# Kernel optimization log

Hardware: AMD Instinct MI355X
Metric: run time of the kernel (lower is better)

## Reference

```python
import jax, jax.numpy as jnp
import numpy as np

B, T, D_IN = 512, 128, 256
H1, H2 = 1024, 1024
LABEL_DIM = 3


def _lstm_layer(x, W, U, b):
    """Run one keras-LSTMCell layer over x: [T, B, D_in] -> [T, B, H].

    Keras gate order is (i, f, g, o); c' = f*c + i*tanh(g); h = o*tanh(c').
    """
    H = U.shape[0]
    batch = x.shape[1]

    def step(carry, xt):
        h, c = carry
        z = xt @ W + h @ U + b  # [B, 4H]
        i, f, g, o = jnp.split(z, 4, axis=-1)
        i = jax.nn.sigmoid(i)
        f = jax.nn.sigmoid(f)
        g = jnp.tanh(g)
        o = jax.nn.sigmoid(o)
        c_new = f * c + i * g
        h_new = o * jnp.tanh(c_new)
        return (h_new, c_new), h_new

    init = (jnp.zeros((batch, H), x.dtype), jnp.zeros((batch, H), x.dtype))
    _, hs = jax.lax.scan(step, init, x)
    return hs  # [T, B, H]


def setup_inputs() -> dict:
    key = jax.random.key(0)
    ks = jax.random.split(key, 10)
    chars = jax.random.normal(ks[0], (B, T, D_IN), dtype=jnp.float32)
    # sequence lengths in [1, T] so sequence_length - 1 is a valid index
    sequence_length = jax.random.randint(ks[1], (B,), 1, T + 1)
    s = 0.05
    W1 = jax.random.normal(ks[2], (D_IN, 4 * H1), dtype=jnp.float32) * s
    U1 = jax.random.normal(ks[3], (H1, 4 * H1), dtype=jnp.float32) * s
    b1 = jnp.zeros((4 * H1,), dtype=jnp.float32)
    W2 = jax.random.normal(ks[4], (H1, 4 * H2), dtype=jnp.float32) * s
    U2 = jax.random.normal(ks[5], (H2, 4 * H2), dtype=jnp.float32) * s
    b2 = jnp.zeros((4 * H2,), dtype=jnp.float32)
    Wd = jax.random.normal(ks[6], (H2, LABEL_DIM), dtype=jnp.float32) * s
    bd = jnp.zeros((LABEL_DIM,), dtype=jnp.float32)
    return {"chars": chars, "sequence_length": sequence_length,
            "W1": W1, "U1": U1, "b1": b1,
            "W2": W2, "U2": U2, "b2": b2,
            "Wd": Wd, "bd": bd}


def reference(chars, sequence_length, W1, U1, b1, W2, U2, b2, Wd, bd):
    # chars: [B, T, 256] -> time-major [T, B, 256]
    x = jnp.transpose(chars, (1, 0, 2))
    x = _lstm_layer(x, W1, U1, b1)          # [T, B, H1]
    x = _lstm_layer(x, W2, U2, b2)          # [T, B, H2]
    # gather the hidden state at the last valid timestep of each sequence
    batch = chars.shape[0]
    hidden = x[sequence_length - 1, jnp.arange(batch)]  # [B, H2]
    return jax.nn.relu(hidden @ Wd + bd)    # [B, label_dim]
```

## Files before the change

kernel.cpp:

```cpp
#include <hip/hip_runtime.h>
#include <hip/hip_bf16.h>


typedef __hip_bfloat16 bf16;
typedef __attribute__((ext_vector_type(8))) short bfrag8;
typedef __attribute__((ext_vector_type(4))) float accf4;

#define BATCH 512
#define TSTEPS 128
#define DIN 256
#define H 1024
#define NG 4096

__device__ __forceinline__ float sigm(float x) { return 1.0f / (1.0f + __expf(-x)); }
__device__ __forceinline__ float tanh_f(float x) {
    float a = fabsf(x);
    float e = __expf(-2.0f * a);
    float t = (1.0f - e) / (1.0f + e);
    return x < 0.0f ? -t : t;
}
__device__ __forceinline__ unsigned short bfr16(float x) {
    bf16 h = __float2bfloat16(x);
    return *(unsigned short*)&h;
}
__device__ __forceinline__ void gll16(const void* g, void* l) {
    __builtin_amdgcn_global_load_lds(
        (const __attribute__((address_space(1))) unsigned int*)g,
        (__attribute__((address_space(3))) unsigned int*)l, 16, 0, 0);
}

__global__ void k_repack(const float* __restrict__ W, const float* __restrict__ U,
                         bf16* __restrict__ Bp, int KIN)
{
    __shared__ float tile[128][65];
    int kt = blockIdx.x, nt = blockIdx.y;
    int lane = threadIdx.x;
    int n = nt * 64 + lane;
    int orig = ((n >> 4) & 3) * 1024 + (n >> 7) * 32 + ((n >> 6) & 1) * 16 + (n & 15);
    for (int j = 0; j < 128; ++j) {
        int k = kt * 128 + j;
        tile[j][lane] = (k < KIN) ? W[(size_t)k * NG + orig]
                                  : U[(size_t)(k - KIN) * NG + orig];
    }
    __syncthreads();
    for (int u = 0; u < 16; ++u) {
        int cid = u * 64 + lane;
        int nloc = cid >> 4;
        int pos = cid & 15;
        int nn = nt * 64 + nloc;
        int kc = pos ^ (nn & 7);
        alignas(16) unsigned short pk[8];
        #pragma unroll
        for (int jj = 0; jj < 8; ++jj) pk[jj] = bfr16(tile[kc * 8 + jj][nloc]);
        *(int4*)(Bp + ((size_t)kt * NG + nn) * 128 + pos * 8) = *(int4*)pk;
    }
}

__global__ void k_sort(const int* __restrict__ seqlen, int* __restrict__ perm,
                       int* __restrict__ cnt)
{
    __shared__ int hist[129];
    __shared__ int base[129];
    __shared__ int cur[129];
    int tid = threadIdx.x;
    if (tid < 129) { hist[tid] = 0; cur[tid] = 0; }
    __syncthreads();
    int len = seqlen[tid];
    atomicAdd(&hist[len], 1);
    __syncthreads();
    if (tid == 0) {
        int acc = 0;
        for (int l = 128; l >= 1; --l) { base[l] = acc; acc += hist[l]; }
        base[0] = acc;
    }
    __syncthreads();
    int pos = base[len] + atomicAdd(&cur[len], 1);
    perm[pos] = tid;
    if (tid < 128) cnt[tid] = base[tid];
}

struct StepJob {
    const float* Xf;
    const bf16* A0;
    const bf16* A1;
    const bf16* Bp;
    const float* bias;
    float* C;
    bf16* Hout;
    float* hidden;
    const int* seqlen;
    const int* perm;
    const int* cnt;
    int xstride;
    int ksplit;
    int KT;
    int t;
};

__global__ __launch_bounds__(256, 2) void k_step(StepJob j0, StepJob j1)
{
    __shared__ __align__(16) bf16 Alds[64 * 128];
    __shared__ __align__(16) bf16 Blds[128 * 128];

    int jidx = blockIdx.x >> 8;
    const StepJob jb = jidx ? j1 : j0;
    int bi = blockIdx.x & 255;
    int xcd = bi & 7;
    int s = bi >> 3;
    int btr = s >> 2;
    int btile = jidx ? (7 - btr) : btr;
    int ntile = ((s & 3) << 3) | xcd;
    int b0 = btile * 64;
    if (b0 >= jb.cnt[jb.t]) return;

    int tid = threadIdx.x;
    int wv = tid >> 6, lane = tid & 63;
    int n0 = ntile * 128;
    int mw = (wv & 1) * 32;
    int nw = (wv >> 1) * 64;
    int c = lane & 15, q = lane >> 4;

    const accf4 zero4 = {0.f, 0.f, 0.f, 0.f};
    accf4 acc[2][4];
    #pragma unroll
    for (int i = 0; i < 2; ++i)
        #pragma unroll
        for (int j = 0; j < 4; ++j) acc[i][j] = zero4;

    for (int kt = 0; kt < jb.KT; ++kt) {
        int k0 = kt << 7;
        if (jb.Xf && k0 < jb.ksplit) {
            #pragma unroll
            for (int uu = 0; uu < 4; ++uu) {
                int u = uu * 256 + tid;
                int r = u >> 4;
                int pos = u & 15;
                int kc = pos ^ (r & 7);
                const float* src = jb.Xf + (size_t)jb.perm[b0 + r] * jb.xstride + k0 + kc * 8;
                float4 va = *(const float4*)src;
                float4 vb = *(const float4*)(src + 4);
                alignas(16) unsigned short pk[8];
                pk[0] = bfr16(va.x); pk[1] = bfr16(va.y);
                pk[2] = bfr16(va.z); pk[3] = bfr16(va.w);
                pk[4] = bfr16(vb.x); pk[5] = bfr16(vb.y);
                pk[6] = bfr16(vb.z); pk[7] = bfr16(vb.w);
                *(int4*)((char*)Alds + u * 16) = *(int4*)pk;
            }
        } else {
            const bf16* Asrc; int kk0;
            if (k0 < jb.ksplit) { Asrc = jb.A0; kk0 = k0; }
            else                { Asrc = jb.A1; kk0 = k0 - jb.ksplit; }
            #pragma unroll
            for (int cc = 0; cc < 4; ++cc) {
                int ob = wv * 4096 + cc * 1024;
                int o = ob + lane * 16;
                int r = o >> 8;
                const char* g = (const char*)Asrc + (size_t)(b0 + r) * (H * 2) + kk0 * 2 + (o & 255);
                gll16(g, (char*)Alds + ob);
            }
        }
        const char* Bg = (const char*)jb.Bp + ((size_t)kt * NG + n0) * 256;
        #pragma unroll
        for (int cc = 0; cc < 8; ++cc) {
            int ob = wv * 8192 + cc * 1024;
            gll16(Bg + ob + lane * 16, (char*)Blds + ob);
        }
        __syncthreads();
        #pragma unroll
        for (int kk = 0; kk < 128; kk += 32) {
            int kc = (kk >> 3) + q;
            int ra = mw + c;
            int pa = (kc ^ (ra & 7)) << 3;
            bfrag8 af0 = *(const bfrag8*)(Alds + ra * 128 + pa);
            bfrag8 af1 = *(const bfrag8*)(Alds + (ra + 16) * 128 + pa);
            #pragma unroll
            for (int nt = 0; nt < 4; ++nt) {
                int nn = nw + nt * 16 + c;
                bfrag8 bfv = *(const bfrag8*)(Blds + nn * 128 + ((kc ^ (nn & 7)) << 3));
                acc[0][nt] = __builtin_amdgcn_mfma_f32_16x16x32_bf16(af0, bfv, acc[0][nt], 0, 0, 0);
                acc[1][nt] = __builtin_amdgcn_mfma_f32_16x16x32_bf16(af1, bfv, acc[1][nt], 0, 0, 0);
            }
        }
        __syncthreads();
    }

    int hcol = ntile * 32 + (wv >> 1) * 16 + c;
    float bi_ = jb.bias[hcol],         bf_ = jb.bias[H + hcol];
    float bg_ = jb.bias[2 * H + hcol], bo_ = jb.bias[3 * H + hcol];
    int seg = hcol & ~127;
    int kc_ = (hcol & 127) >> 3;
    int jl = hcol & 7;
    #pragma unroll
    for (int mt = 0; mt < 2; ++mt) {
        #pragma unroll
        for (int reg = 0; reg < 4; ++reg) {
            int b = b0 + mw + mt * 16 + q * 4 + reg;
            float ig = sigm(acc[mt][0][reg] + bi_);
            float fg = sigm(acc[mt][1][reg] + bf_);
            float gv = tanh_f(acc[mt][2][reg] + bg_);
            float og = sigm(acc[mt][3][reg] + bo_);
            size_t ci = (size_t)b * H + hcol;
            float cv = fg * jb.C[ci] + ig * gv;
            jb.C[ci] = cv;
            float h = og * tanh_f(cv);
            jb.Hout[(size_t)b * H + seg + ((kc_ ^ (b & 7)) << 3) + jl] = __float2bfloat16(h);
            if (jb.hidden) {
                int pb = jb.perm[b];
                if (jb.seqlen[pb] - 1 == jb.t)
                    jb.hidden[(size_t)pb * H + hcol] = h;
            }
        }
    }
}

__global__ void k_final(const float* __restrict__ hidden, const float* __restrict__ Wd,
                        const float* __restrict__ bd, float* __restrict__ out)
{
    int b = blockIdx.x;
    int l = threadIdx.x;
    float p0 = 0.f, p1 = 0.f, p2 = 0.f;
    for (int jj = l; jj < H; jj += 64) {
        float hv = hidden[(size_t)b * H + jj];
        p0 += hv * Wd[jj * 3 + 0];
        p1 += hv * Wd[jj * 3 + 1];
        p2 += hv * Wd[jj * 3 + 2];
    }
    #pragma unroll
    for (int off = 32; off > 0; off >>= 1) {
        p0 += __shfl_down(p0, off);
        p1 += __shfl_down(p1, off);
        p2 += __shfl_down(p2, off);
    }
    if (l == 0) {
        out[b * 3 + 0] = fmaxf(p0 + bd[0], 0.f);
        out[b * 3 + 1] = fmaxf(p1 + bd[1], 0.f);
        out[b * 3 + 2] = fmaxf(p2 + bd[2], 0.f);
    }
}

extern "C" void kernel_launch(void* const* d_in, const int* in_sizes, int n_in,
                              void* d_out, int out_size, void* d_ws, size_t ws_size,
                              hipStream_t stream)
{
    const float* chars = (const float*)d_in[0];
    const int* seqlen  = (const int*)d_in[1];
    const float* W1 = (const float*)d_in[2];
    const float* U1 = (const float*)d_in[3];
    const float* b1 = (const float*)d_in[4];
    const float* W2 = (const float*)d_in[5];
    const float* U2 = (const float*)d_in[6];
    const float* b2 = (const float*)d_in[7];
    const float* Wd = (const float*)d_in[8];
    const float* bd = (const float*)d_in[9];
    float* out = (float*)d_out;

    char* ws = (char*)d_ws;
    size_t off = 0;
    bf16* Bp1 = (bf16*)(ws + off); off += (size_t)10 * NG * 128 * 2;
    bf16* Bp2 = (bf16*)(ws + off); off += (size_t)16 * NG * 128 * 2;
    bf16* h1  = (bf16*)(ws + off); off += (size_t)2 * BATCH * H * 2;
    bf16* h2  = (bf16*)(ws + off); off += (size_t)2 * BATCH * H * 2;
    float* c1 = (float*)(ws + off); off += (size_t)BATCH * H * 4;
    float* c2 = (float*)(ws + off); off += (size_t)BATCH * H * 4;
    float* hidden = (float*)(ws + off); off += (size_t)BATCH * H * 4;
    int* perm = (int*)(ws + off); off += BATCH * 4;
    int* cntA = (int*)(ws + off); off += TSTEPS * 4;
    if (ws_size < off) return;

    hipMemsetAsync(h1, 0, (size_t)2 * BATCH * H * 2, stream);
    hipMemsetAsync(h2, 0, (size_t)2 * BATCH * H * 2, stream);
    hipMemsetAsync(c1, 0, (size_t)BATCH * H * 4, stream);
    hipMemsetAsync(c2, 0, (size_t)BATCH * H * 4, stream);

    k_repack<<<dim3(10, 64), 64, 0, stream>>>(W1, U1, Bp1, 256);
    k_repack<<<dim3(16, 64), 64, 0, stream>>>(W2, U2, Bp2, 1024);
    k_sort<<<1, 512, 0, stream>>>(seqlen, perm, cntA);

    const size_t HS = (size_t)BATCH * H;

    auto mkL1 = [&](int s) {
        StepJob J;
        J.Xf = chars + (size_t)s * DIN;  J.xstride = TSTEPS * DIN;
        J.A0 = nullptr;
        J.A1 = h1 + (size_t)((s + 1) & 1) * HS;
        J.Bp = Bp1; J.bias = b1; J.C = c1;
        J.Hout = h1 + (size_t)(s & 1) * HS;
        J.hidden = nullptr; J.seqlen = nullptr;
        J.perm = perm; J.cnt = cntA;
        J.ksplit = 256; J.KT = 10; J.t = s;
        return J;
    };
    auto mkL2 = [&](int s) {
        StepJob J;
        J.Xf = nullptr; J.xstride = 0;
        J.A0 = h1 + (size_t)(s & 1) * HS;
        J.A1 = h2 + (size_t)((s + 1) & 1) * HS;
        J.Bp = Bp2; J.bias = b2; J.C = c2;
        J.Hout = h2 + (size_t)(s & 1) * HS;
        J.hidden = hidden; J.seqlen = seqlen;
        J.perm = perm; J.cnt = cntA;
        J.ksplit = 1024; J.KT = 16; J.t = s;
        return J;
    };

    StepJob first = mkL1(0);
    k_step<<<256, 256, 0, stream>>>(first, first);
    for (int t = 0; t < TSTEPS - 1; ++t) {
        k_step<<<512, 256, 0, stream>>>(mkL2(t), mkL1(t + 1));
    }
    StepJob last = mkL2(TSTEPS - 1);
    k_step<<<256, 256, 0, stream>>>(last, last);
    k_final<<<512, 64, 0, stream>>>(hidden, Wd, bd, out);
}
```

Before: 3.756 ms.

## Replace per-timestep kernel launches with a persistent kernel and grid barrier

The 129 per-step launches become one persistent kernel of 512 blocks. Each block loops over timesteps and synchronises with the others through an atomic-counter grid barrier backed by agent-scope fences. This removes launch overhead and the kernel-boundary drain between steps. It depends on all 512 blocks being co-resident (two blocks per CU under the launch bounds), adds spin-wait cost, and has a guard that can break out of the barrier, which risks correctness if it fires.

```diff
diff --git a/kernel.cpp b/kernel.cpp
--- a/kernel.cpp
+++ b/kernel.cpp
@@ -11,6 +11,7 @@
 #define DIN 256
 #define H 1024
 #define NG 4096
+#define NBLK 512
 
 __device__ __forceinline__ float sigm(float x) { return 1.0f / (1.0f + __expf(-x)); }
 __device__ __forceinline__ float tanh_f(float x) {
@@ -90,36 +91,17 @@
     float* hidden;
     const int* seqlen;
     const int* perm;
-    const int* cnt;
     int xstride;
     int ksplit;
     int KT;
     int t;
 };
 
-__global__ __launch_bounds__(256, 2) void k_step(StepJob j0, StepJob j1)
-{
-    __shared__ __align__(16) bf16 Alds[64 * 128];
-    __shared__ __align__(16) bf16 Blds[128 * 128];
-
-    int jidx = blockIdx.x >> 8;
-    const StepJob jb = jidx ? j1 : j0;
-    int bi = blockIdx.x & 255;
-    int xcd = bi & 7;
-    int s = bi >> 3;
-    int btr = s >> 2;
-    int btile = jidx ? (7 - btr) : btr;
-    int ntile = ((s & 3) << 3) | xcd;
-    int b0 = btile * 64;
-    if (b0 >= jb.cnt[jb.t]) return;
-
-    int tid = threadIdx.x;
-    int wv = tid >> 6, lane = tid & 63;
-    int n0 = ntile * 128;
-    int mw = (wv & 1) * 32;
-    int nw = (wv >> 1) * 64;
-    int c = lane & 15, q = lane >> 4;
-
+__device__ __forceinline__ void step_body(
+    const StepJob& jb, bf16* Alds, bf16* Blds,
+    int b0, int n0, int ntile, int tid, int wv, int lane,
+    int mw, int nw, int c, int q, bool is_l2)
+{
     const accf4 zero4 = {0.f, 0.f, 0.f, 0.f};
     accf4 acc[2][4];
     #pragma unroll
@@ -204,11 +186,101 @@
             jb.C[ci] = cv;
             float h = og * tanh_f(cv);
             jb.Hout[(size_t)b * H + seg + ((kc_ ^ (b & 7)) << 3) + jl] = __float2bfloat16(h);
-            if (jb.hidden) {
+            if (is_l2) {
                 int pb = jb.perm[b];
                 if (jb.seqlen[pb] - 1 == jb.t)
                     jb.hidden[(size_t)pb * H + hcol] = h;
             }
+        }
+    }
+}
+
+struct PersistArgs {
+    const float* chars;
+    const int* seqlen;
+    const float* b1; const float* b2;
+    const bf16* Bp1; const bf16* Bp2;
+    float* c1; float* c2;
+    bf16* h1; bf16* h2;
+    float* hidden;
+    const int* perm; const int* cnt;
+    unsigned* bar;
+};
+
+__global__ __launch_bounds__(256, 2) void k_persist(PersistArgs P)
+{
+    __shared__ __align__(16) bf16 Alds[64 * 128];
+    __shared__ __align__(16) bf16 Blds[128 * 128];
+
+    int jidx = blockIdx.x >> 8;
+    int bi = blockIdx.x & 255;
+    int xcd = bi & 7;
+    int sl = bi >> 3;
+    int btr = sl >> 2;
+    int btile = jidx ? (7 - btr) : btr;
+    int ntile = ((sl & 3) << 3) | xcd;
+    int b0 = btile * 64;
+
+    int tid = threadIdx.x;
+    int wv = tid >> 6, lane = tid & 63;
+    int n0 = ntile * 128;
+    int mw = (wv & 1) * 32;
+    int nw = (wv >> 1) * 64;
+    int c = lane & 15, q = lane >> 4;
+    const size_t HS = (size_t)BATCH * H;
+
+    StepJob J;
+    J.perm = P.perm;
+    if (jidx == 1) {
+        J.Bp = P.Bp1; J.bias = P.b1; J.C = P.c1;
+        J.hidden = nullptr; J.seqlen = nullptr;
+        J.xstride = TSTEPS * DIN; J.ksplit = 256; J.KT = 10;
+    } else {
+        J.Bp = P.Bp2; J.bias = P.b2; J.C = P.c2;
+        J.hidden = P.hidden; J.seqlen = P.seqlen;
+        J.xstride = 0; J.ksplit = 1024; J.KT = 16;
+    }
+
+    for (int s = 0; s <= TSTEPS; ++s) {
+        bool active;
+        if (jidx == 0) {
+            active = (s >= 1);
+            int t = s - 1;
+            J.t = t;
+            J.Xf = nullptr;
+            J.A0 = P.h1 + (size_t)(t & 1) * HS;
+            J.A1 = P.h2 + (size_t)((t + 1) & 1) * HS;
+            J.Hout = P.h2 + (size_t)(t & 1) * HS;
+        } else {
+            active = (s < TSTEPS);
+            int t = s;
+            J.t = t;
+            J.Xf = P.chars + (size_t)t * DIN;
+            J.A0 = nullptr;
+            J.A1 = P.h1 + (size_t)((t + 1) & 1) * HS;
+            J.Hout = P.h1 + (size_t)(t & 1) * HS;
+        }
+        if (active && b0 < P.cnt[J.t]) {
+            step_body(J, Alds, Blds, b0, n0, ntile, tid, wv, lane, mw, nw, c, q,
+                      jidx == 0);
+        }
+
+        if (s < TSTEPS) {
+            __builtin_amdgcn_fence(__ATOMIC_RELEASE, "agent");
+            __syncthreads();
+            if (tid == 0) {
+                __hip_atomic_fetch_add(P.bar, 1u, __ATOMIC_RELAXED,
+                                       __HIP_MEMORY_SCOPE_AGENT);
+                unsigned target = (unsigned)(s + 1) * NBLK;
+                int guard = 0;
+                while (__hip_atomic_load(P.bar, __ATOMIC_RELAXED,
+                                         __HIP_MEMORY_SCOPE_AGENT) < target) {
+                    __builtin_amdgcn_s_sleep(1);
+                    if (++guard > 100000) break;
+                }
+            }
+            __syncthreads();
+            __builtin_amdgcn_fence(__ATOMIC_ACQUIRE, "agent");
         }
     }
 }
@@ -265,50 +337,29 @@
     float* hidden = (float*)(ws + off); off += (size_t)BATCH * H * 4;
     int* perm = (int*)(ws + off); off += BATCH * 4;
     int* cntA = (int*)(ws + off); off += TSTEPS * 4;
+    unsigned* bar = (unsigned*)(ws + off); off += 256;
     if (ws_size < off) return;
 
     hipMemsetAsync(h1, 0, (size_t)2 * BATCH * H * 2, stream);
     hipMemsetAsync(h2, 0, (size_t)2 * BATCH * H * 2, stream);
     hipMemsetAsync(c1, 0, (size_t)BATCH * H * 4, stream);
     hipMemsetAsync(c2, 0, (size_t)BATCH * H * 4, stream);
+    hipMemsetAsync(bar, 0, 256, stream);
 
     k_repack<<<dim3(10, 64), 64, 0, stream>>>(W1, U1, Bp1, 256);
     k_repack<<<dim3(16, 64), 64, 0, stream>>>(W2, U2, Bp2, 1024);
     k_sort<<<1, 512, 0, stream>>>(seqlen, perm, cntA);
 
-    const size_t HS = (size_t)BATCH * H;
-
-    auto mkL1 = [&](int s) {
-        StepJob J;
-        J.Xf = chars + (size_t)s * DIN;  J.xstride = TSTEPS * DIN;
-        J.A0 = nullptr;
-        J.A1 = h1 + (size_t)((s + 1) & 1) * HS;
-        J.Bp = Bp1; J.bias = b1; J.C = c1;
-        J.Hout = h1 + (size_t)(s & 1) * HS;
-        J.hidden = nullptr; J.seqlen = nullptr;
-        J.perm = perm; J.cnt = cntA;
-        J.ksplit = 256; J.KT = 10; J.t = s;
-        return J;
-    };
-    auto mkL2 = [&](int s) {
-        StepJob J;
-        J.Xf = nullptr; J.xstride = 0;
-        J.A0 = h1 + (size_t)(s & 1) * HS;
-        J.A1 = h2 + (size_t)((s + 1) & 1) * HS;
-        J.Bp = Bp2; J.bias = b2; J.C = c2;
-        J.Hout = h2 + (size_t)(s & 1) * HS;
-        J.hidden = hidden; J.seqlen = seqlen;
-        J.perm = perm; J.cnt = cntA;
-        J.ksplit = 1024; J.KT = 16; J.t = s;
-        return J;
-    };
-
-    StepJob first = mkL1(0);
-    k_step<<<256, 256, 0, stream>>>(first, first);
-    for (int t = 0; t < TSTEPS - 1; ++t) {
-        k_step<<<512, 256, 0, stream>>>(mkL2(t), mkL1(t + 1));
-    }
-    StepJob last = mkL2(TSTEPS - 1);
-    k_step<<<256, 256, 0, stream>>>(last, last);
+    PersistArgs P;
+    P.chars = chars; P.seqlen = seqlen;
+    P.b1 = b1; P.b2 = b2;
+    P.Bp1 = Bp1; P.Bp2 = Bp2;
+    P.c1 = c1; P.c2 = c2;
+    P.h1 = h1; P.h2 = h2;
+    P.hidden = hidden;
+    P.perm = perm; P.cnt = cntA;
+    P.bar = bar;
+    k_persist<<<dim3(NBLK), dim3(256), 0, stream>>>(P);
+
     k_final<<<512, 64, 0, stream>>>(hidden, Wd, bd, out);
 }
```

After: 13.46 ms. 3.58x slower.

## Double-buffer B tiles in LDS and prefetch A through registers in step GEMM

Applied to the files above, without the earlier changes.

The k-loop now stages the next B tile into a second LDS buffer and loads the next A tile into registers while MFMAs run on the current tile. The A tile is then written to LDS between barriers. This is meant to overlap global-memory latency with compute instead of loading and then waiting each iteration. It doubles B's LDS footprint, raises register pressure, and swaps direct-to-LDS loads for register round-trips on A.

```diff
diff --git a/kernel.cpp b/kernel.cpp
--- a/kernel.cpp
+++ b/kernel.cpp
@@ -100,16 +100,16 @@
 __global__ __launch_bounds__(256, 2) void k_step(StepJob j0, StepJob j1)
 {
     __shared__ __align__(16) bf16 Alds[64 * 128];
-    __shared__ __align__(16) bf16 Blds[128 * 128];
+    __shared__ __align__(16) bf16 Blds[2 * 128 * 128];
 
     int jidx = blockIdx.x >> 8;
     const StepJob jb = jidx ? j1 : j0;
     int bi = blockIdx.x & 255;
     int xcd = bi & 7;
-    int s = bi >> 3;
-    int btr = s >> 2;
+    int sl = bi >> 3;
+    int btr = sl >> 2;
     int btile = jidx ? (7 - btr) : btr;
-    int ntile = ((s & 3) << 3) | xcd;
+    int ntile = ((sl & 3) << 3) | xcd;
     int b0 = btile * 64;
     if (b0 >= jb.cnt[jb.t]) return;
 
@@ -119,6 +119,7 @@
     int mw = (wv & 1) * 32;
     int nw = (wv >> 1) * 64;
     int c = lane & 15, q = lane >> 4;
+    const int KT = jb.KT;
 
     const accf4 zero4 = {0.f, 0.f, 0.f, 0.f};
     accf4 acc[2][4];
@@ -127,45 +128,86 @@
         #pragma unroll
         for (int j = 0; j < 4; ++j) acc[i][j] = zero4;
 
-    for (int kt = 0; kt < jb.KT; ++kt) {
+    int4 areg0, areg1, areg2, areg3;
+    float4 xr00, xr01, xr10, xr11, xr20, xr21, xr30, xr31;
+
+    auto stageB = [&](int kt, int buf) {
+        const char* Bg = (const char*)jb.Bp + ((size_t)kt * NG + n0) * 256;
+        char* dst = (char*)Blds + buf * 32768;
+        #pragma unroll
+        for (int cc = 0; cc < 8; ++cc) {
+            int ob = wv * 8192 + cc * 1024;
+            gll16(Bg + ob + lane * 16, dst + ob);
+        }
+    };
+    auto issueA = [&](int kt) {
         int k0 = kt << 7;
         if (jb.Xf && k0 < jb.ksplit) {
             #pragma unroll
-            for (int uu = 0; uu < 4; ++uu) {
-                int u = uu * 256 + tid;
+            for (int j = 0; j < 4; ++j) {
+                int u = j * 256 + tid;
                 int r = u >> 4;
-                int pos = u & 15;
-                int kc = pos ^ (r & 7);
+                int kc = (u & 15) ^ (r & 7);
                 const float* src = jb.Xf + (size_t)jb.perm[b0 + r] * jb.xstride + k0 + kc * 8;
                 float4 va = *(const float4*)src;
                 float4 vb = *(const float4*)(src + 4);
+                if (j == 0) { xr00 = va; xr01 = vb; }
+                else if (j == 1) { xr10 = va; xr11 = vb; }
+                else if (j == 2) { xr20 = va; xr21 = vb; }
+                else { xr30 = va; xr31 = vb; }
+            }
+        } else {
+            const bf16* Asrc; int kk0;
+            if (k0 < jb.ksplit) { Asrc = jb.A0; kk0 = k0; }
+            else                { Asrc = jb.A1; kk0 = k0 - jb.ksplit; }
+            const char* gb = (const char*)Asrc + (size_t)b0 * 2048
+                           + (size_t)kk0 * 2 + (tid & 15) * 16;
+            int rr = tid >> 4;
+            areg0 = *(const int4*)(gb + (size_t)(0 * 16 + rr) * 2048);
+            areg1 = *(const int4*)(gb + (size_t)(1 * 16 + rr) * 2048);
+            areg2 = *(const int4*)(gb + (size_t)(2 * 16 + rr) * 2048);
+            areg3 = *(const int4*)(gb + (size_t)(3 * 16 + rr) * 2048);
+        }
+    };
+    auto writeA = [&](int kt) {
+        int k0 = kt << 7;
+        char* dst = (char*)Alds + tid * 16;
+        if (jb.Xf && k0 < jb.ksplit) {
+            #pragma unroll
+            for (int j = 0; j < 4; ++j) {
+                float4 va, vb;
+                if (j == 0) { va = xr00; vb = xr01; }
+                else if (j == 1) { va = xr10; vb = xr11; }
+                else if (j == 2) { va = xr20; vb = xr21; }
+                else { va = xr30; vb = xr31; }
                 alignas(16) unsigned short pk[8];
                 pk[0] = bfr16(va.x); pk[1] = bfr16(va.y);
                 pk[2] = bfr16(va.z); pk[3] = bfr16(va.w);
                 pk[4] = bfr16(vb.x); pk[5] = bfr16(vb.y);
                 pk[6] = bfr16(vb.z); pk[7] = bfr16(vb.w);
-                *(int4*)((char*)Alds + u * 16) = *(int4*)pk;
+                *(int4*)(dst + j * 4096) = *(int4*)pk;
             }
         } else {
-            const bf16* Asrc; int kk0;
-            if (k0 < jb.ksplit) { Asrc = jb.A0; kk0 = k0; }
-            else                { Asrc = jb.A1; kk0 = k0 - jb.ksplit; }
-            #pragma unroll
-            for (int cc = 0; cc < 4; ++cc) {
-                int ob = wv * 4096 + cc * 1024;
-                int o = ob + lane * 16;
-                int r = o >> 8;
-                const char* g = (const char*)Asrc + (size_t)(b0 + r) * (H * 2) + kk0 * 2 + (o & 255);
-                gll16(g, (char*)Alds + ob);
-            }
-        }
-        const char* Bg = (const char*)jb.Bp + ((size_t)kt * NG + n0) * 256;
-        #pragma unroll
-        for (int cc = 0; cc < 8; ++cc) {
-            int ob = wv * 8192 + cc * 1024;
-            gll16(Bg + ob + lane * 16, (char*)Blds + ob);
-        }
-        __syncthreads();
+            *(int4*)(dst + 0 * 4096) = areg0;
+            *(int4*)(dst + 1 * 4096) = areg1;
+            *(int4*)(dst + 2 * 4096) = areg2;
+            *(int4*)(dst + 3 * 4096) = areg3;
+        }
+    };
+
+    stageB(0, 0);
+    issueA(0);
+    __syncthreads();
+    writeA(0);
+    __syncthreads();
+
+    for (int kt = 0; kt < KT; ++kt) {
+        int nb = kt + 1;
+        if (nb < KT) {
+            stageB(nb, nb & 1);
+            issueA(nb);
+        }
+        const bf16* Bcur = Blds + (kt & 1) * 16384;
         #pragma unroll
         for (int kk = 0; kk < 128; kk += 32) {
             int kc = (kk >> 3) + q;
@@ -176,12 +218,16 @@
             #pragma unroll
             for (int nt = 0; nt < 4; ++nt) {
                 int nn = nw + nt * 16 + c;
-                bfrag8 bfv = *(const bfrag8*)(Blds + nn * 128 + ((kc ^ (nn & 7)) << 3));
+                bfrag8 bfv = *(const bfrag8*)(Bcur + nn * 128 + ((kc ^ (nn & 7)) << 3));
                 acc[0][nt] = __builtin_amdgcn_mfma_f32_16x16x32_bf16(af0, bfv, acc[0][nt], 0, 0, 0);
                 acc[1][nt] = __builtin_amdgcn_mfma_f32_16x16x32_bf16(af1, bfv, acc[1][nt], 0, 0, 0);
             }
         }
-        __syncthreads();
+        if (nb < KT) {
+            __syncthreads();
+            writeA(nb);
+            __syncthreads();
+        }
     }
 
     int hcol = ntile * 32 + (wv >> 1) * 16 + c;
@@ -267,10 +313,10 @@
     int* cntA = (int*)(ws + off); off += TSTEPS * 4;
     if (ws_size < off) return;
 
-    hipMemsetAsync(h1, 0, (size_t)2 * BATCH * H * 2, stream);
-    hipMemsetAsync(h2, 0, (size_t)2 * BATCH * H * 2, stream);
-    hipMemsetAsync(c1, 0, (size_t)BATCH * H * 4, stream);
-    hipMemsetAsync(c2, 0, (size_t)BATCH * H * 4, stream);
+    (void)hipMemsetAsync(h1, 0, (size_t)2 * BATCH * H * 2, stream);
+    (void)hipMemsetAsync(h2, 0, (size_t)2 * BATCH * H * 2, stream);
+    (void)hipMemsetAsync(c1, 0, (size_t)BATCH * H * 4, stream);
+    (void)hipMemsetAsync(c2, 0, (size_t)BATCH * H * 4, stream);
 
     k_repack<<<dim3(10, 64), 64, 0, stream>>>(W1, U1, Bp1, 256);
     k_repack<<<dim3(16, 64), 64, 0, stream>>>(W2, U2, Bp2, 1024);
```

Measured after the change: 3.986 ms. 1.06x slower.
